# Performance work log

Hardware: AMD Instinct MI355X
Metric: run time of the kernel (lower is better)

The kernel has to match this reference:

```python
import jax, jax.numpy as jnp
import numpy as np

B, S, DM = 4, 8192, 1024
N_RED = 16384   # tokens merged into their right neighbor
N_SAVE = 16384  # tokens kept; must be divisible by B


def setup_inputs() -> dict:
    key = jax.random.key(0)
    k1, k2, k3, k4 = jax.random.split(key, 4)
    x = jax.random.normal(k1, (B, S, DM), dtype=jnp.float32)
    W = jax.random.normal(k2, (DM, DM), dtype=jnp.float32) * (1.0 / np.sqrt(DM))
    ids_to_reduce = jax.random.randint(k3, (N_RED,), 0, B * S - 1, dtype=jnp.int64)
    ids_to_save = jax.random.randint(k4, (N_SAVE,), 0, B * S, dtype=jnp.int64)
    return {"x": x, "W": W, "ids_to_save": ids_to_save, "ids_to_reduce": ids_to_reduce}


def reference(x, W, ids_to_save, ids_to_reduce):
    batch_size, _, dm = x.shape
    xf = x.reshape(-1, dm)                       # [B*S, dm]
    reduced = xf[ids_to_reduce]                  # gather  [N_RED, dm]
    transformed = (reduced @ W.T).astype(jnp.float32)  # Linear, no bias
    xf = xf.at[ids_to_reduce + 1].add(transformed)     # scatter-add into right neighbor
    saved = xf[ids_to_save]                      # gather  [N_SAVE, dm]
    return saved.reshape(batch_size, -1, dm)     # [B, N_SAVE//B, dm]
```

## Files before the change

### kernel.cpp

```cpp
#include <hip/hip_runtime.h>

#define DM    1024
#define NTOK  32768
#define NRED  16384
#define NSAVE 16384
#define MMAX  16384

typedef __attribute__((ext_vector_type(8))) short bf16x8;
typedef __attribute__((ext_vector_type(4))) float f32x4;

__device__ __forceinline__ ushort f2bf(float f) {
    union { float f; unsigned u; } v; v.f = f;
    unsigned r = (v.u + 0x7FFF + ((v.u >> 16) & 1)) >> 16;
    return (ushort)r;
}
__device__ __forceinline__ float bf2f(ushort u) {
    union { unsigned u; float f; } v; v.u = ((unsigned)u) << 16;
    return v.f;
}

__global__ __launch_bounds__(256) void setup_kernel(const float* __restrict__ W,
                                                    ushort* __restrict__ Wb,
                                                    int* __restrict__ cnt,
                                                    int* __restrict__ need,
                                                    int* __restrict__ counter) {
    int t = blockIdx.x * 256 + threadIdx.x;
    float4 v = ((const float4*)W)[t];
    ushort4 o;
    o.x = f2bf(v.x); o.y = f2bf(v.y); o.z = f2bf(v.z); o.w = f2bf(v.w);
    ((ushort4*)Wb)[t] = o;
    if (t < NTOK) { cnt[t] = 0; need[t] = 0; }
    if (t == 0) *counter = 0;
}

__global__ __launch_bounds__(256) void prep_kernel(const int* __restrict__ red,
                                                   const int* __restrict__ sav,
                                                   int* __restrict__ cnt,
                                                   int* __restrict__ need) {
    int j = blockIdx.x * 256 + threadIdx.x;
    if (j >= NRED) return;
    atomicAdd(&cnt[red[j]], 1);
    int s = sav[j];
    if (s > 0) need[s - 1] = 1;
}

__global__ __launch_bounds__(256) void compact_kernel(const int* __restrict__ cnt,
                                                      const int* __restrict__ need,
                                                      int* __restrict__ inv,
                                                      int* __restrict__ list,
                                                      int* __restrict__ counter) {
    int t = blockIdx.x * 256 + threadIdx.x;
    if (t >= NTOK) return;
    if (need[t] && cnt[t] > 0) {
        int pos = atomicAdd(counter, 1);
        inv[t] = pos;
        list[pos] = t;
    }
}

__global__ __launch_bounds__(256) void convx_kernel(const float* __restrict__ X,
                                                    const int* __restrict__ list,
                                                    const int* __restrict__ counter,
                                                    ushort* __restrict__ Xb) {
    const int M = *counter;
    for (int r = blockIdx.x; r < M; r += gridDim.x) {
        int src = list[r];
        float4 v = ((const float4*)(X + (size_t)src * DM))[threadIdx.x];
        ushort4 o;
        o.x = f2bf(v.x); o.y = f2bf(v.y); o.z = f2bf(v.z); o.w = f2bf(v.w);
        ((ushort4*)(Xb + (size_t)r * DM))[threadIdx.x] = o;
    }
}

__global__ __launch_bounds__(256) void gemm_kernel(const ushort* __restrict__ Xb,
                                                   const ushort* __restrict__ Wb,
                                                   const int* __restrict__ counter,
                                                   ushort* __restrict__ Tb) {
    const int M = *counter;
    const int m0 = blockIdx.x * 64;
    if (m0 >= M) return;
    const int n0 = blockIdx.y * 64;

    __shared__ char lds[65536];

    const int tid  = threadIdx.x;
    const int lane = tid & 63;
    const int w    = tid >> 6;

    const ushort* a_src[4];
    const ushort* b_src[4];
#pragma unroll
    for (int i = 0; i < 4; ++i) {
        int q   = w * 256 + i * 64 + lane;
        int row = q >> 4;
        int c   = (q & 15) ^ (row & 7);
        int ar  = m0 + row; if (ar >= M) ar = M - 1;
        a_src[i] = Xb + (size_t)ar * DM + c * 8;
        b_src[i] = Wb + (size_t)(n0 + row) * DM + c * 8;
    }

#define STAGE(buf, k0) do {                                                          \
    char* _base = lds + (buf) * 32768 + w * 4096;                                    \
    _Pragma("unroll")                                                                \
    for (int _i = 0; _i < 4; ++_i) {                                                 \
        __builtin_amdgcn_global_load_lds(                                            \
            (const __attribute__((address_space(1))) unsigned*)(a_src[_i] + (k0)),   \
            (__attribute__((address_space(3))) unsigned*)(_base + _i * 1024),        \
            16, 0, 0);                                                               \
        __builtin_amdgcn_global_load_lds(                                            \
            (const __attribute__((address_space(1))) unsigned*)(b_src[_i] + (k0)),   \
            (__attribute__((address_space(3))) unsigned*)(_base + 16384 + _i * 1024),\
            16, 0, 0);                                                               \
    }                                                                                \
} while (0)

    int aoff[4], boff[4];
#pragma unroll
    for (int f = 0; f < 4; ++f) {
        int row = f * 16 + (lane & 15);
        int c   = w * 4 + (lane >> 4);
        int cp  = c ^ (row & 7);
        aoff[f] = row * 256 + cp * 16;
        boff[f] = row * 256 + cp * 16;
    }

    f32x4 acc[4][4] = {};

    STAGE(0, 0);
#pragma unroll
    for (int t = 0; t < 8; ++t) {
        const int cur = t & 1;
        if (t < 7) {
            STAGE(cur ^ 1, (t + 1) * 128);
            asm volatile("s_waitcnt vmcnt(8)" ::: "memory");
        } else {
            asm volatile("s_waitcnt vmcnt(0)" ::: "memory");
        }
        __builtin_amdgcn_s_barrier();

        const char* A = lds + cur * 32768;
        const char* B = A + 16384;
        bf16x8 af[4], bfr[4];
#pragma unroll
        for (int i = 0; i < 4; ++i) af[i]  = *(const bf16x8*)(A + aoff[i]);
#pragma unroll
        for (int j = 0; j < 4; ++j) bfr[j] = *(const bf16x8*)(B + boff[j]);
#pragma unroll
        for (int i = 0; i < 4; ++i)
#pragma unroll
            for (int j = 0; j < 4; ++j)
                acc[i][j] = __builtin_amdgcn_mfma_f32_16x16x32_bf16(af[i], bfr[j], acc[i][j], 0, 0, 0);

        asm volatile("s_waitcnt lgkmcnt(0)" ::: "memory");
        __builtin_amdgcn_s_barrier();
    }

#pragma unroll
    for (int fm = 0; fm < 4; ++fm)
#pragma unroll
        for (int fn = 0; fn < 4; ++fn) {
            int F = fm * 4 + fn;
            *(f32x4*)(lds + w * 16384 + lane * 256 + ((F ^ (lane & 15)) << 4)) = acc[fm][fn];
        }
    __syncthreads();

#pragma unroll
    for (int fn = 0; fn < 4; ++fn) {
        int F = w * 4 + fn;
        f32x4 s = {0.f, 0.f, 0.f, 0.f};
#pragma unroll
        for (int sw = 0; sw < 4; ++sw)
            s += *(const f32x4*)(lds + sw * 16384 + lane * 256 + ((F ^ (lane & 15)) << 4));
        int n  = n0 + fn * 16 + (lane & 15);
        int mb = m0 + w * 16 + (lane >> 4) * 4;
#pragma unroll
        for (int r = 0; r < 4; ++r)
            if (mb + r < M) Tb[(size_t)(mb + r) * DM + n] = f2bf(s[r]);
    }
#undef STAGE
}

__global__ __launch_bounds__(256) void out_kernel(const float* __restrict__ X,
                                                  const ushort* __restrict__ Tb,
                                                  const int* __restrict__ sav,
                                                  const int* __restrict__ cnt,
                                                  const int* __restrict__ inv,
                                                  float* __restrict__ out) {
    int r = blockIdx.x;
    int d = threadIdx.x;
    int s = sav[r];
    const float4* xr = (const float4*)(X + (size_t)s * DM);
    float4 v = xr[d];
    if (s > 0) {
        int t = s - 1;
        int c = cnt[t];
        if (c > 0) {
            float fc = (float)c;
            const ushort4* tr = (const ushort4*)(Tb + (size_t)inv[t] * DM);
            ushort4 wv = tr[d];
            v.x += fc * bf2f(wv.x); v.y += fc * bf2f(wv.y);
            v.z += fc * bf2f(wv.z); v.w += fc * bf2f(wv.w);
        }
    }
    ((float4*)out)[(size_t)r * (DM / 4) + d] = v;
}

extern "C" void kernel_launch(void* const* d_in, const int* in_sizes, int n_in,
                              void* d_out, int out_size, void* d_ws, size_t ws_size,
                              hipStream_t stream) {
    const float* X   = (const float*)d_in[0];
    const float* W   = (const float*)d_in[1];
    const int*   sav = (const int*)d_in[2];
    const int*   red = (const int*)d_in[3];
    float* out = (float*)d_out;

    char* ws = (char*)d_ws;
    int* counter = (int*)ws;
    int* cnt  = counter + 64;
    int* need = cnt + NTOK;
    int* inv  = need + NTOK;
    int* list = inv + NTOK;
    ushort* Wb = (ushort*)(ws + (1 << 19));
    ushort* Xb = (ushort*)(ws + (4 << 20));
    ushort* Tb = (ushort*)(ws + (36u << 20));

    setup_kernel<<<DM * DM / 4 / 256, 256, 0, stream>>>(W, Wb, cnt, need, counter);
    prep_kernel<<<NRED / 256, 256, 0, stream>>>(red, sav, cnt, need);
    compact_kernel<<<NTOK / 256, 256, 0, stream>>>(cnt, need, inv, list, counter);
    convx_kernel<<<2048, 256, 0, stream>>>(X, list, counter, Xb);

    dim3 ggrid(MMAX / 64, DM / 64);
    gemm_kernel<<<ggrid, 256, 0, stream>>>(Xb, Wb, counter, Tb);

    out_kernel<<<NSAVE, 256, 0, stream>>>(X, Tb, sav, cnt, inv, out);
}
```

Baseline: 73.69 us.

## Replace split-K 4-wave GEMM tile with single-wave full-K tile

```diff
diff --git a/kernel.cpp b/kernel.cpp
--- a/kernel.cpp
+++ b/kernel.cpp
@@ -63,121 +63,106 @@
                                                     const int* __restrict__ counter,
                                                     ushort* __restrict__ Xb) {
     const int M = *counter;
-    for (int r = blockIdx.x; r < M; r += gridDim.x) {
-        int src = list[r];
-        float4 v = ((const float4*)(X + (size_t)src * DM))[threadIdx.x];
+    const int Mpad = (M + 63) & ~63;
+    for (int r = blockIdx.x; r < Mpad; r += gridDim.x) {
         ushort4 o;
-        o.x = f2bf(v.x); o.y = f2bf(v.y); o.z = f2bf(v.z); o.w = f2bf(v.w);
+        if (r < M) {
+            int src = list[r];
+            float4 v = ((const float4*)(X + (size_t)src * DM))[threadIdx.x];
+            o.x = f2bf(v.x); o.y = f2bf(v.y); o.z = f2bf(v.z); o.w = f2bf(v.w);
+        } else {
+            o.x = 0; o.y = 0; o.z = 0; o.w = 0;
+        }
         ((ushort4*)(Xb + (size_t)r * DM))[threadIdx.x] = o;
     }
 }
 
-__global__ __launch_bounds__(256) void gemm_kernel(const ushort* __restrict__ Xb,
-                                                   const ushort* __restrict__ Wb,
-                                                   const int* __restrict__ counter,
-                                                   ushort* __restrict__ Tb) {
+__global__ __launch_bounds__(64) void gemm_kernel(const ushort* __restrict__ Xb,
+                                                  const ushort* __restrict__ Wb,
+                                                  const int* __restrict__ counter,
+                                                  ushort* __restrict__ Tb) {
     const int M = *counter;
     const int m0 = blockIdx.x * 64;
     if (m0 >= M) return;
     const int n0 = blockIdx.y * 64;
 
-    __shared__ char lds[65536];
-
-    const int tid  = threadIdx.x;
-    const int lane = tid & 63;
-    const int w    = tid >> 6;
-
-    const ushort* a_src[4];
-    const ushort* b_src[4];
-#pragma unroll
-    for (int i = 0; i < 4; ++i) {
-        int q   = w * 256 + i * 64 + lane;
-        int row = q >> 4;
-        int c   = (q & 15) ^ (row & 7);
-        int ar  = m0 + row; if (ar >= M) ar = M - 1;
-        a_src[i] = Xb + (size_t)ar * DM + c * 8;
-        b_src[i] = Wb + (size_t)(n0 + row) * DM + c * 8;
-    }
-
-#define STAGE(buf, k0) do {                                                          \
-    char* _base = lds + (buf) * 32768 + w * 4096;                                    \
-    _Pragma("unroll")                                                                \
-    for (int _i = 0; _i < 4; ++_i) {                                                 \
-        __builtin_amdgcn_global_load_lds(                                            \
-            (const __attribute__((address_space(1))) unsigned*)(a_src[_i] + (k0)),   \
-            (__attribute__((address_space(3))) unsigned*)(_base + _i * 1024),        \
-            16, 0, 0);                                                               \
-        __builtin_amdgcn_global_load_lds(                                            \
-            (const __attribute__((address_space(1))) unsigned*)(b_src[_i] + (k0)),   \
-            (__attribute__((address_space(3))) unsigned*)(_base + 16384 + _i * 1024),\
-            16, 0, 0);                                                               \
-    }                                                                                \
+    __shared__ char lds[32768];
+
+    const int l = threadIdx.x;
+    const int srow   = l >> 3;
+    const int schunk = (l & 7) ^ (srow & 7);
+    const ushort* aS = Xb + (size_t)(m0 + srow) * DM + schunk * 8;
+    const ushort* bS = Wb + (size_t)(n0 + srow) * DM + schunk * 8;
+
+#define STAGE(buf, k0) do {                                                         \
+    char* _d = lds + (buf) * 16384;                                                 \
+    _Pragma("unroll")                                                               \
+    for (int _i = 0; _i < 8; ++_i) {                                                \
+        __builtin_amdgcn_global_load_lds(                                           \
+            (const __attribute__((address_space(1))) unsigned*)(aS + (k0) + _i * 8 * DM), \
+            (__attribute__((address_space(3))) unsigned*)(_d + _i * 1024), 16, 0, 0);     \
+        __builtin_amdgcn_global_load_lds(                                           \
+            (const __attribute__((address_space(1))) unsigned*)(bS + (k0) + _i * 8 * DM), \
+            (__attribute__((address_space(3))) unsigned*)(_d + 8192 + _i * 1024), 16, 0, 0); \
+    }                                                                               \
 } while (0)
 
-    int aoff[4], boff[4];
+    const int kgrp = l >> 4;
+    const int r16  = l & 15;
+    int off[4][2];
 #pragma unroll
     for (int f = 0; f < 4; ++f) {
-        int row = f * 16 + (lane & 15);
-        int c   = w * 4 + (lane >> 4);
-        int cp  = c ^ (row & 7);
-        aoff[f] = row * 256 + cp * 16;
-        boff[f] = row * 256 + cp * 16;
+        int row = f * 16 + r16;
+#pragma unroll
+        for (int kk = 0; kk < 2; ++kk)
+            off[f][kk] = row * 128 + (((kk * 4 + kgrp) ^ (row & 7)) * 16);
     }
 
     f32x4 acc[4][4] = {};
 
     STAGE(0, 0);
 #pragma unroll
-    for (int t = 0; t < 8; ++t) {
-        const int cur = t & 1;
-        if (t < 7) {
-            STAGE(cur ^ 1, (t + 1) * 128);
-            asm volatile("s_waitcnt vmcnt(8)" ::: "memory");
+    for (int t = 0; t < 16; ++t) {
+        const char* base = lds + (t & 1) * 16384;
+        if (t < 15) {
+            asm volatile("s_waitcnt lgkmcnt(0)" ::: "memory");
+            __builtin_amdgcn_sched_barrier(0);
+            STAGE((t & 1) ^ 1, (t + 1) * 64);
+            asm volatile("s_waitcnt vmcnt(16)" ::: "memory");
+            __builtin_amdgcn_sched_barrier(0);
         } else {
             asm volatile("s_waitcnt vmcnt(0)" ::: "memory");
-        }
-        __builtin_amdgcn_s_barrier();
-
-        const char* A = lds + cur * 32768;
-        const char* B = A + 16384;
-        bf16x8 af[4], bfr[4];
-#pragma unroll
-        for (int i = 0; i < 4; ++i) af[i]  = *(const bf16x8*)(A + aoff[i]);
-#pragma unroll
-        for (int j = 0; j < 4; ++j) bfr[j] = *(const bf16x8*)(B + boff[j]);
-#pragma unroll
-        for (int i = 0; i < 4; ++i)
-#pragma unroll
-            for (int j = 0; j < 4; ++j)
-                acc[i][j] = __builtin_amdgcn_mfma_f32_16x16x32_bf16(af[i], bfr[j], acc[i][j], 0, 0, 0);
-
-        asm volatile("s_waitcnt lgkmcnt(0)" ::: "memory");
-        __builtin_amdgcn_s_barrier();
-    }
-
-#pragma unroll
-    for (int fm = 0; fm < 4; ++fm)
+            __builtin_amdgcn_sched_barrier(0);
+        }
+#pragma unroll
+        for (int kk = 0; kk < 2; ++kk) {
+            bf16x8 af[4], bfr[4];
+#pragma unroll
+            for (int f = 0; f < 4; ++f) af[f]  = *(const bf16x8*)(base + off[f][kk]);
+#pragma unroll
+            for (int f = 0; f < 4; ++f) bfr[f] = *(const bf16x8*)(base + 8192 + off[f][kk]);
+#pragma unroll
+            for (int i = 0; i < 4; ++i)
+#pragma unroll
+                for (int j = 0; j < 4; ++j)
+                    acc[i][j] = __builtin_amdgcn_mfma_f32_16x16x32_bf16(af[i], bfr[j], acc[i][j], 0, 0, 0);
+        }
+    }
+#undef STAGE
+
+#pragma unroll
+    for (int fm = 0; fm < 4; ++fm) {
+        int mbase = m0 + fm * 16 + kgrp * 4;
 #pragma unroll
         for (int fn = 0; fn < 4; ++fn) {
-            int F = fm * 4 + fn;
-            *(f32x4*)(lds + w * 16384 + lane * 256 + ((F ^ (lane & 15)) << 4)) = acc[fm][fn];
-        }
-    __syncthreads();
-
-#pragma unroll
-    for (int fn = 0; fn < 4; ++fn) {
-        int F = w * 4 + fn;
-        f32x4 s = {0.f, 0.f, 0.f, 0.f};
-#pragma unroll
-        for (int sw = 0; sw < 4; ++sw)
-            s += *(const f32x4*)(lds + sw * 16384 + lane * 256 + ((F ^ (lane & 15)) << 4));
-        int n  = n0 + fn * 16 + (lane & 15);
-        int mb = m0 + w * 16 + (lane >> 4) * 4;
-#pragma unroll
-        for (int r = 0; r < 4; ++r)
-            if (mb + r < M) Tb[(size_t)(mb + r) * DM + n] = f2bf(s[r]);
-    }
-#undef STAGE
+            int n = n0 + fn * 16 + r16;
+#pragma unroll
+            for (int r = 0; r < 4; ++r) {
+                int m = mbase + r;
+                if (m < M) Tb[(size_t)m * DM + n] = f2bf(acc[fm][fn][r]);
+            }
+        }
+    }
 }
 
 __global__ __launch_bounds__(256) void out_kernel(const float* __restrict__ X,
@@ -230,7 +215,7 @@
     convx_kernel<<<2048, 256, 0, stream>>>(X, list, counter, Xb);
 
     dim3 ggrid(MMAX / 64, DM / 64);
-    gemm_kernel<<<ggrid, 256, 0, stream>>>(Xb, Wb, counter, Tb);
+    gemm_kernel<<<ggrid, 64, 0, stream>>>(Xb, Wb, counter, Tb);
 
     out_kernel<<<NSAVE, 256, 0, stream>>>(X, Tb, sav, cnt, inv, out);
 }
```

Result: slower. 76.49 us (+3.8%).
